# Kernel tuning notes

Hardware: AMD Instinct MI355X
Metric: run time of the kernel (lower is better)

The kernel has to match this reference:

```python
import jax, jax.numpy as jnp
import numpy as np
from jax import lax

WS = 8       # RSA window size
HEADS = 8    # GSA heads
EPS_LN = 1e-5

def conv1x1(x, w):  # x:(b,c,h,w), w:(o,c)
    return jnp.einsum('bchw,oc->bohw', x, w)

def dwconv3x3(x, w):  # w:(c,1,3,3) depthwise
    return lax.conv_general_dilated(x, w, (1, 1), ((1, 1), (1, 1)),
                                    dimension_numbers=('NCHW', 'OIHW', 'NCHW'),
                                    feature_group_count=x.shape[1])

def layernorm(x, w, b):  # WithBias LayerNorm over channel dim
    mu = x.mean(axis=1, keepdims=True)
    var = ((x - mu) ** 2).mean(axis=1, keepdims=True)
    return (x - mu) / jnp.sqrt(var + EPS_LN) * w[None, :, None, None] + b[None, :, None, None]

def l2norm(x):  # F.normalize(dim=-1)
    n = jnp.sqrt(jnp.sum(x * x, axis=-1, keepdims=True))
    return x / jnp.maximum(n, 1e-12)

def window_part(x, ws):  # (b,c,H,W) -> (b,nwin,ws*ws,c)
    b, c, H, W = x.shape
    x = x.reshape(b, c, H // ws, ws, W // ws, ws)
    x = x.transpose(0, 2, 4, 3, 5, 1)
    return x.reshape(b, (H // ws) * (W // ws), ws * ws, c)

def window_merge(x, ws, H, W):  # inverse of window_part
    b, nwin, _, c = x.shape
    x = x.reshape(b, H // ws, W // ws, ws, ws, c)
    x = x.transpose(0, 5, 1, 3, 2, 4)
    return x.reshape(b, c, H, W)

def rsa(x, qkv_w, dw_w, proj_w, temp):
    b, c, H, W = x.shape
    sh = WS // 2  # torch: roll by -wsize//2 = -4
    x_ = jnp.roll(x, (-sh, -sh), axis=(2, 3))
    qkv = dwconv3x3(conv1x1(x_, qkv_w), dw_w)
    q, k, v = jnp.split(qkv, 3, axis=1)
    q = l2norm(window_part(q, WS))
    k = l2norm(window_part(k, WS))
    v = window_part(v, WS)
    # attn[c,d] = sum_p q[p,c] k[p,d]; relu instead of softmax
    attn = jax.nn.relu(jnp.einsum('bnpc,bnpd->bncd', q, k) * temp[0, 0, 0])
    out = jnp.einsum('bnpc,bncd->bnpd', v, attn)
    out = window_merge(out, WS, H, W)
    out = jnp.roll(out, (sh, sh), axis=(2, 3))
    return conv1x1(out, proj_w), attn

def gsa(x, qkv_w, dw_w, proj_w, temp):
    b, c, H, W = x.shape
    cp = c // HEADS
    qkv = dwconv3x3(conv1x1(x, qkv_w), dw_w)
    q, k, v = jnp.split(qkv, 3, axis=1)
    heads = lambda t: t.reshape(b, HEADS, cp, H * W)
    q = l2norm(heads(q)); k = l2norm(heads(k)); v = heads(v)
    attn = jax.nn.relu(jnp.einsum('bhcn,bhdn->bhcd', q, k) * temp[0, 0, 0])
    out = jnp.einsum('bhcd,bhdn->bhcn', attn, v)  # (b,head,cp,HW)
    # rearrange 'b head c hw -> b (head c) h w' then 'b (head c) h w -> b (c head) h w'
    y = out.reshape(b, HEADS, cp, H, W).transpose(0, 2, 1, 3, 4).reshape(b, c, H, W)
    return conv1x1(y, proj_w), attn

def ffn(x, in_w, dw_w, out_w):  # Restormer gated-dconv FFN, bias=False
    h2 = dwconv3x3(conv1x1(x, in_w), dw_w)
    x1, x2 = jnp.split(h2, 2, axis=1)
    return conv1x1(jax.nn.gelu(x1, approximate=False) * x2, out_w)


def setup_inputs() -> dict:
    key = jax.random.key(0)
    B, C, H, W = 8, 64, 128, 128
    HID = int(C * 2.66)  # 170
    ks = jax.random.split(key, 20)
    g = lambda k, shp, s: (jax.random.normal(k, shp, dtype=jnp.float32) * s)
    d = {
        'x': g(ks[0], (B, C, H, W), 1.0),
        'ln_s0_w': jnp.ones((C,), jnp.float32), 'ln_s0_b': jnp.zeros((C,), jnp.float32),
        'ln_s2_w': jnp.ones((C,), jnp.float32), 'ln_s2_b': jnp.zeros((C,), jnp.float32),
        'rsa_qkv_w': g(ks[1], (3 * C, C), 0.05), 'rsa_dw_w': g(ks[2], (3 * C, 1, 3, 3), 0.1),
        'rsa_proj_w': g(ks[3], (C, C), 0.05), 'rsa_temp': jnp.ones((1, 1, 1), jnp.float32),
        'ffd_s_in_w': g(ks[4], (2 * HID, C), 0.05), 'ffd_s_dw_w': g(ks[5], (2 * HID, 1, 3, 3), 0.1),
        'ffd_s_out_w': g(ks[6], (C, HID), 0.05),
        'ln_c0_w': jnp.ones((C,), jnp.float32), 'ln_c0_b': jnp.zeros((C,), jnp.float32),
        'ln_c2_w': jnp.ones((C,), jnp.float32), 'ln_c2_b': jnp.zeros((C,), jnp.float32),
        'gsa_qkv_w': g(ks[7], (3 * C, C), 0.05), 'gsa_dw_w': g(ks[8], (3 * C, 1, 3, 3), 0.1),
        'gsa_proj_w': g(ks[9], (C, C), 0.05), 'gsa_temp': jnp.ones((1, 1, 1), jnp.float32),
        'ffd_c_in_w': g(ks[10], (2 * HID, C), 0.05), 'ffd_c_dw_w': g(ks[11], (2 * HID, 1, 3, 3), 0.1),
        'ffd_c_out_w': g(ks[12], (C, HID), 0.05),
    }
    return d


def reference(x, ln_s0_w, ln_s0_b, ln_s2_w, ln_s2_b,
              rsa_qkv_w, rsa_dw_w, rsa_proj_w, rsa_temp,
              ffd_s_in_w, ffd_s_dw_w, ffd_s_out_w,
              ln_c0_w, ln_c0_b, ln_c2_w, ln_c2_b,
              gsa_qkv_w, gsa_dw_w, gsa_proj_w, gsa_temp,
              ffd_c_in_w, ffd_c_dw_w, ffd_c_out_w):
    # FDT block, shared_depth=1 (i==0 branches only)
    x_, _ = rsa(layernorm(x, ln_s0_w, ln_s0_b), rsa_qkv_w, rsa_dw_w, rsa_proj_w, rsa_temp)
    x = ffn(layernorm(x_ + x, ln_s2_w, ln_s2_b), ffd_s_in_w, ffd_s_dw_w, ffd_s_out_w) + x_
    x_, _ = gsa(layernorm(x, ln_c0_w, ln_c0_b), gsa_qkv_w, gsa_dw_w, gsa_proj_w, gsa_temp)
    x = ffn(layernorm(x_ + x, ln_c2_w, ln_c2_b), ffd_c_in_w, ffd_c_dw_w, ffd_c_out_w) + x_
    return x
```

## Files before the change

kernel.cpp:

```cpp
#include <hip/hip_runtime.h>
#include <hip/hip_bf16.h>
#include <math.h>

#define DI __device__ __forceinline__

constexpr int B = 8, C = 64, H = 128, W = 128, N = H * W;
constexpr int HID = 170;
constexpr int QKVC = 3 * C;

typedef _Float16 half8 __attribute__((ext_vector_type(8)));
typedef _Float16 half4v __attribute__((ext_vector_type(4)));
typedef float f32x4 __attribute__((ext_vector_type(4)));

extern "C" __device__ _Float16 __ocml_exp_f16(_Float16);

DI half8 gelu_gate_h8(half8 a, half8 g) {
    const _Float16 k = (_Float16)0.044715f;
    const _Float16 c = (_Float16)1.5957691f;
    half8 a2 = a * a;
    half8 t = a * ((_Float16)1.f + k * a2);
    half8 o;
#pragma unroll
    for (int i = 0; i < 8; ++i) {
        _Float16 e = __ocml_exp_f16((_Float16)(-c * t[i]));
        o[i] = (_Float16)(a[i] / ((_Float16)1.f + e) * g[i]);
    }
    return o;
}

DI void wpack_dev(const float* __restrict__ Wm, const float* __restrict__ lnsc,
                  int OREAL, int KREAL, int KT, _Float16* __restrict__ out,
                  int f, int l)
{
    int mt = f / KT, kt = f % KT;
    int row = mt * 16 + (l & 15);
    int col0 = kt * 32 + (l >> 4) * 8;
    half8 v;
#pragma unroll
    for (int i = 0; i < 8; ++i) {
        int col = col0 + i;
        float w = (row < OREAL && col < KREAL) ? Wm[row * KREAL + col] : 0.f;
        if (lnsc && col < KREAL) w *= lnsc[col];
        v[i] = (_Float16)w;
    }
    *(half8*)(out + (size_t)f * 512 + l * 8) = v;
}

DI void wbias_dev(const float* __restrict__ Wm, const float* __restrict__ lnb,
                  int OREAL, int OPAD, float* __restrict__ biasv, int blk, int l)
{
    int o = blk * 64 + l;
    if (o >= OPAD) return;
    float s = 0.f;
    if (o < OREAL) {
#pragma unroll
        for (int c = 0; c < 64; ++c) s += Wm[o * 64 + c] * lnb[c];
    }
    biasv[o] = s;
}

__global__ __launch_bounds__(64) void prep_kernel(
    const float* rsa_qkv_w, const float* ln_s0_w, const float* ln_s0_b,
    const float* gsa_qkv_w, const float* ln_c0_w, const float* ln_c0_b,
    const float* ffs_in_w,  const float* ln_s2_w, const float* ln_s2_b,
    const float* ffc_in_w,  const float* ln_c2_w, const float* ln_c2_b,
    const float* ffs_out_w, const float* ffc_out_w, const float* rsa_proj_w,
    _Float16* wp_rsa, _Float16* wp_gsa, _Float16* wp_fsi, _Float16* wp_fci,
    _Float16* wp_fso, _Float16* wp_fco, _Float16* wp_rsap,
    float* wb_rsa, float* wb_gsa, float* wb_fsi, float* wb_fci)
{
    int bid = blockIdx.x, l = threadIdx.x;
    if      (bid < 24)  wpack_dev(rsa_qkv_w, ln_s0_w, 192, 64, 2, wp_rsa, bid, l);
    else if (bid < 48)  wpack_dev(gsa_qkv_w, ln_c0_w, 192, 64, 2, wp_gsa, bid - 24, l);
    else if (bid < 96)  wpack_dev(ffs_in_w,  ln_s2_w, 340, 64, 2, wp_fsi, bid - 48, l);
    else if (bid < 144) wpack_dev(ffc_in_w,  ln_c2_w, 340, 64, 2, wp_fci, bid - 96, l);
    else if (bid < 168) wpack_dev(ffs_out_w, nullptr, 64, 170, 6, wp_fso, bid - 144, l);
    else if (bid < 192) wpack_dev(ffc_out_w, nullptr, 64, 170, 6, wp_fco, bid - 168, l);
    else if (bid < 200) wpack_dev(rsa_proj_w, nullptr, 64, 64, 2, wp_rsap, bid - 192, l);
    else if (bid < 203) wbias_dev(rsa_qkv_w, ln_s0_b, 192, 192, wb_rsa, bid - 200, l);
    else if (bid < 206) wbias_dev(gsa_qkv_w, ln_c0_b, 192, 192, wb_gsa, bid - 203, l);
    else if (bid < 212) wbias_dev(ffs_in_w, ln_s2_b, 340, 384, wb_fsi, bid - 206, l);
    else                wbias_dev(ffc_in_w, ln_c2_b, 340, 384, wb_fci, bid - 212, l);
}

__global__ __launch_bounds__(256, 1) void xpose_kernel(
    const float* __restrict__ x, _Float16* __restrict__ xT)
{
    __shared__ _Float16 tile[64][72];
    int blk = blockIdx.x;
    int b = blk >> 8, tb = blk & 255;
    int n0 = tb * 64;
    int t = threadIdx.x;
    {
        int ch = t >> 2, seg = t & 3;
        const float* xp = x + ((size_t)b * 64 + ch) * N + n0 + seg * 16;
#pragma unroll
        for (int jj = 0; jj < 4; ++jj) {
            f32x4 v = *(const f32x4*)(xp + jj * 4);
#pragma unroll
            for (int k = 0; k < 4; ++k)
                tile[seg * 16 + jj * 4 + k][ch] = (_Float16)v[k];
        }
    }
    __syncthreads();
    {
        int px = t >> 2, part = t & 3;
        half8 h0 = *(const half8*)&tile[px][part * 16];
        half8 h1 = *(const half8*)&tile[px][part * 16 + 8];
        _Float16* op = xT + ((size_t)b * N + n0 + px) * 64 + part * 16;
        *(half8*)op = h0;
        *(half8*)(op + 8) = h1;
    }
}

template<int MT, int OREAL, bool ADDIN>
__global__ __launch_bounds__(512, 1) void lngemm_kernel(
    const _Float16* __restrict__ Xp, const _Float16* __restrict__ Rp,
    const float* __restrict__ biasv,
    const _Float16* __restrict__ Wp, _Float16* __restrict__ outp)
{
    __shared__ _Float16 stash[4][MT][16][66];
    int t = threadIdx.x, lane = t & 63, wv = t >> 6;
    int mg = wv & 3, ph = wv >> 2;
    int pbase = blockIdx.x * 64;
    int b = pbase >> 14, nb = pbase & (N - 1);
    int g = lane >> 4, lm = lane & 15;
    int krow0 = g * 8;

    half8 a[MT][2];
    const _Float16* wb = Wp + (size_t)(mg * MT * 2) * 512 + lane * 8;
#pragma unroll
    for (int mt = 0; mt < MT; ++mt)
#pragma unroll
        for (int kt = 0; kt < 2; ++kt)
            a[mt][kt] = *(const half8*)(wb + (mt * 2 + kt) * 512);

    int rowbase = mg * (MT * 16);
    const float* bp = biasv + rowbase + g * 4;

    const _Float16* xb = Xp + (size_t)b * N * 64;
    const _Float16* ab = ADDIN ? (Rp + (size_t)b * N * 64) : nullptr;

#pragma unroll
    for (int cg2 = 0; cg2 < 2; ++cg2) {
        int cg = ph * 2 + cg2;
        int col = nb + cg * 16 + lm;
        const _Float16* xp = xb + (size_t)col * 64;
        half8 h0 = *(const half8*)(xp + krow0);
        half8 h1 = *(const half8*)(xp + 32 + krow0);
        float vv[2][8];
        float sm = 0.f, ss = 0.f;
        if (ADDIN) {
            const _Float16* ap = ab + (size_t)col * 64;
            half8 r0 = *(const half8*)(ap + krow0);
            half8 r1 = *(const half8*)(ap + 32 + krow0);
#pragma unroll
            for (int i = 0; i < 8; ++i) {
                float v0 = (float)h0[i] + (float)r0[i];
                float v1 = (float)h1[i] + (float)r1[i];
                vv[0][i] = v0; vv[1][i] = v1;
                sm += v0 + v1; ss += v0 * v0 + v1 * v1;
            }
        } else {
#pragma unroll
            for (int i = 0; i < 8; ++i) {
                float v0 = (float)h0[i], v1 = (float)h1[i];
                vv[0][i] = v0; vv[1][i] = v1;
                sm += v0 + v1; ss += v0 * v0 + v1 * v1;
            }
        }
        sm += __shfl_xor(sm, 16); ss += __shfl_xor(ss, 16);
        sm += __shfl_xor(sm, 32); ss += __shfl_xor(ss, 32);
        float mu = sm * (1.0f / 64.0f);
        float var = ss * (1.0f / 64.0f) - mu * mu;
        float rstd = rsqrtf(var + 1e-5f);
        half8 bf[2];
#pragma unroll
        for (int kt = 0; kt < 2; ++kt)
#pragma unroll
            for (int i = 0; i < 8; ++i)
                bf[kt][i] = (_Float16)((vv[kt][i] - mu) * rstd);

        f32x4 acc[MT];
#pragma unroll
        for (int mt = 0; mt < MT; ++mt) acc[mt] = *(const f32x4*)(bp + mt * 16);
#pragma unroll
        for (int kt = 0; kt < 2; ++kt)
#pragma unroll
            for (int mt = 0; mt < MT; ++mt)
                acc[mt] = __builtin_amdgcn_mfma_f32_16x16x32_f16(a[mt][kt], bf[kt], acc[mt], 0, 0, 0);

#pragma unroll
        for (int mt = 0; mt < MT; ++mt)
#pragma unroll
            for (int r = 0; r < 4; ++r)
                stash[mg][mt][g * 4 + r][cg * 16 + lm] = (_Float16)acc[mt][r];
    }
    __syncthreads();

    int tid128 = ph * 64 + lane;
    int row = tid128 >> 3, ch8 = tid128 & 7;
#pragma unroll
    for (int mt = 0; mt < MT; ++mt) {
        int orow = rowbase + mt * 16 + row;
        if ((4 * MT * 16 == OREAL) || orow < OREAL) {
            half8 v0 = *(const half8*)&stash[mg][mt][row][ch8 * 8];
            *(half8*)(outp + ((size_t)b * OREAL + orow) * N + nb + ch8 * 8) = v0;
        }
    }
}

template<int MT, int KT, int MG, int NSTRIP, int CIN, int OREAL, int XROWS,
         bool PBW, bool OUT32, bool RESID>
__global__ __launch_bounds__(256, 1) void gemm_kernel(
    const _Float16* __restrict__ X, const _Float16* __restrict__ Wp,
    const _Float16* __restrict__ resid, void* __restrict__ outv)
{
    constexpr int PG = 4 / MG;
    constexpr int PPB = PG * 16 * NSTRIP;
    int t = threadIdx.x;
    int lane = t & 63, wv = t >> 6;
    int mg = wv % MG, pg = wv / MG;
    int pbase = blockIdx.x * PPB;
    int b = pbase >> 14, nb = pbase & (N - 1);

    half8 a[MT][KT];
    const _Float16* wb = Wp + ((size_t)(PBW ? b * (MG * MT * KT) : 0) + mg * MT * KT) * 512 + lane * 8;
#pragma unroll
    for (int mt = 0; mt < MT; ++mt)
#pragma unroll
        for (int kt = 0; kt < KT; ++kt)
            a[mt][kt] = *(const half8*)(wb + (mt * KT + kt) * 512);

    const _Float16* xb = X + (size_t)b * XROWS * N;
    int krow0 = (lane >> 4) * 8;

    for (int s = 0; s < NSTRIP; ++s) {
        int col = nb + (s * PG + pg) * 16 + (lane & 15);
        const _Float16* xp = xb + col;
        half8 bf[KT];
#pragma unroll
        for (int kt = 0; kt < KT; ++kt)
#pragma unroll
            for (int i = 0; i < 8; ++i) {
                int c = kt * 32 + krow0 + i;
                if (KT * 32 <= CIN || c < CIN) bf[kt][i] = xp[(size_t)c * N];
                else bf[kt][i] = (_Float16)0.f;
            }
        f32x4 acc[MT];
#pragma unroll
        for (int mt = 0; mt < MT; ++mt) acc[mt] = (f32x4){0.f, 0.f, 0.f, 0.f};
#pragma unroll
        for (int kt = 0; kt < KT; ++kt)
#pragma unroll
            for (int mt = 0; mt < MT; ++mt)
                acc[mt] = __builtin_amdgcn_mfma_f32_16x16x32_f16(a[mt][kt], bf[kt], acc[mt], 0, 0, 0);

        int orow0 = mg * (MT * 16) + (lane >> 4) * 4;
#pragma unroll
        for (int mt = 0; mt < MT; ++mt) {
            int ob0 = orow0 + mt * 16;
            half4v res;
            if constexpr (RESID)
                res = *(const half4v*)(resid + ((size_t)b * N + col) * 64 + ob0);
            if constexpr (OUT32) {
#pragma unroll
                for (int r = 0; r < 4; ++r) {
                    float vv = acc[mt][r];
                    if constexpr (RESID) vv += (float)res[r];
                    ((float*)outv)[((size_t)b * OREAL + ob0 + r) * N + col] = vv;
                }
            } else {
                half4v h;
#pragma unroll
                for (int r = 0; r < 4; ++r) {
                    float vv = acc[mt][r];
                    if constexpr (RESID) vv += (float)res[r];
                    h[r] = (_Float16)vv;
                }
                *(half4v*)((_Float16*)outv + ((size_t)b * N + col) * 64 + ob0) = h;
            }
        }
    }
}

template<bool ROLLWM>
__global__ __launch_bounds__(256, 1) void dw16_kernel(
    const _Float16* __restrict__ in, const float* __restrict__ w,
    _Float16* __restrict__ out)
{
    int bc = blockIdx.y;
    int c = bc % 192;
    int n0 = (blockIdx.x * 256 + threadIdx.x) * 8;
    int y = n0 >> 7, x0 = n0 & 127;
    const _Float16* ib = in + (size_t)bc * N;
    const float* wr = w + c * 9;
    _Float16 wh[9];
#pragma unroll
    for (int i = 0; i < 9; ++i) wh[i] = (_Float16)wr[i];

    half8 acc = {0, 0, 0, 0, 0, 0, 0, 0};
#pragma unroll
    for (int r = 0; r < 3; ++r) {
        int yy = y - 1 + r;
        if (yy < 0 || yy > 127) continue;
        half8 sL, m, sR;
        if (!ROLLWM) {
            const _Float16* rp = ib + yy * W + x0;
            m = *(const half8*)rp;
            half8 pv = {0, 0, 0, 0, 0, 0, 0, 0};
            half8 nv = {0, 0, 0, 0, 0, 0, 0, 0};
            pv[7] = (x0 > 0) ? rp[-1] : (_Float16)0.f;
            nv[0] = (x0 < 120) ? rp[8] : (_Float16)0.f;
            sL = __builtin_shufflevector(pv, m, 7, 8, 9, 10, 11, 12, 13, 14);
            sR = __builtin_shufflevector(m, nv, 1, 2, 3, 4, 5, 6, 7, 8);
        } else {
            int sy = (yy + 4) & 127;
            const _Float16* rp = ib + sy * W;
            if (x0 <= 112) {
                half8 b0 = *(const half8*)(rp + x0);
                half8 b1 = *(const half8*)(rp + x0 + 8);
                sL = __builtin_shufflevector(b0, b1, 3, 4, 5, 6, 7, 8, 9, 10);
                m  = __builtin_shufflevector(b0, b1, 4, 5, 6, 7, 8, 9, 10, 11);
                sR = __builtin_shufflevector(b0, b1, 5, 6, 7, 8, 9, 10, 11, 12);
                if (x0 == 0) sL[0] = (_Float16)0.f;
            } else {
                _Float16 tmp[10];
#pragma unroll
                for (int j = 0; j < 10; ++j) {
                    int xx = 119 + j;
                    tmp[j] = (xx <= 127) ? rp[(xx + 4) & 127] : (_Float16)0.f;
                }
#pragma unroll
                for (int j = 0; j < 8; ++j) { sL[j] = tmp[j]; m[j] = tmp[j + 1]; sR[j] = tmp[j + 2]; }
            }
        }
        acc += sL * wh[r * 3 + 0] + m * wh[r * 3 + 1] + sR * wh[r * 3 + 2];
    }
    if (ROLLWM) {
        int win = ((y >> 3) << 4) | (x0 >> 3);
        int p = (y & 7) << 3;
        *(half8*)(out + (size_t)bc * N + win * 64 + p) = acc;
    } else {
        *(half8*)(out + (size_t)bc * N + n0) = acc;
    }
}

__global__ __launch_bounds__(256, 3) void rsa_win_kernel(
    const _Float16* __restrict__ qkv, const float* __restrict__ temp_p,
    const _Float16* __restrict__ pwp, _Float16* __restrict__ out)
{
    __shared__ _Float16 qT[64][72];
    __shared__ _Float16 kT[64][72];
    __shared__ _Float16 vP[64][76];
    __shared__ _Float16 aT[64][76];
    __shared__ _Float16 oP[64][76];
    __shared__ float tnorm[128];
    __shared__ _Float16 wsc[64];
    int blk = blockIdx.x, b = blk >> 8, win = blk & 255;
    int t = threadIdx.x, lane = t & 63, wv = t >> 6;
    int g = lane >> 4, lm = lane & 15;

    half8 pa0 = *(const half8*)(pwp + (size_t)(wv * 2 + 0) * 512 + lane * 8);
    half8 pa1 = *(const half8*)(pwp + (size_t)(wv * 2 + 1) * 512 + lane * 8);

    const _Float16* base = qkv + (size_t)b * QKVC * N + win * 64;
    {
        int c = t >> 2, q0 = (t & 3) * 16;
        const _Float16* pq = base + (size_t)c * N + q0;
        half8 a0 = *(const half8*)(pq);
        half8 a1 = *(const half8*)(pq + 8);
        *(half8*)&qT[c][q0] = a0;
        *(half8*)&qT[c][q0 + 8] = a1;
        const _Float16* pk = base + (size_t)(64 + c) * N + q0;
        half8 b0 = *(const half8*)(pk);
        half8 b1 = *(const half8*)(pk + 8);
        *(half8*)&kT[c][q0] = b0;
        *(half8*)&kT[c][q0 + 8] = b1;
        const _Float16* pv = base + (size_t)(128 + c) * N + q0;
        half8 v0 = *(const half8*)(pv);
        half8 v1 = *(const half8*)(pv + 8);
#pragma unroll
        for (int j = 0; j < 8; ++j) vP[q0 + j][c] = v0[j];
#pragma unroll
        for (int j = 0; j < 8; ++j) vP[q0 + 8 + j][c] = v1[j];
    }
    __syncthreads();
    if (t < 128) {
        int p = t & 63;
        float s = 0.f;
        if (t < 64) {
#pragma unroll
            for (int c = 0; c < 64; ++c) { float a = (float)qT[c][p]; s += a * a; }
        } else {
#pragma unroll
            for (int c = 0; c < 64; ++c) { float a = (float)kT[c][p]; s += a * a; }
        }
        tnorm[t] = s;
    }
    __syncthreads();
    if (t < 64) {
        float r = temp_p[0] / (fmaxf(sqrtf(tnorm[t]), 1e-12f) * fmaxf(sqrtf(tnorm[64 + t]), 1e-12f));
        wsc[t] = (_Float16)r;
    }
    __syncthreads();

    {
        half8 aq0 = *(const half8*)&qT[wv * 16 + lm][g * 8];
        half8 aq1 = *(const half8*)&qT[wv * 16 + lm][32 + g * 8];
        half8 ws0 = *(const half8*)&wsc[g * 8];
        half8 ws1 = *(const half8*)&wsc[32 + g * 8];
#pragma unroll
        for (int nt = 0; nt < 4; ++nt) {
            int d = nt * 16 + lm;
            half8 bk0 = *(const half8*)&kT[d][g * 8] * ws0;
            half8 bk1 = *(const half8*)&kT[d][32 + g * 8] * ws1;
            f32x4 acc = {0.f, 0.f, 0.f, 0.f};
            acc = __builtin_amdgcn_mfma_f32_16x16x32_f16(aq0, bk0, acc, 0, 0, 0);
            acc = __builtin_amdgcn_mfma_f32_16x16x32_f16(aq1, bk1, acc, 0, 0, 0);
#pragma unroll
            for (int r = 0; r < 4; ++r)
                aT[wv * 16 + g * 4 + r][d] = (_Float16)fmaxf(acc[r], 0.f);
        }
    }
    __syncthreads();

    {
        half8 a20, a21;
#pragma unroll
        for (int i = 0; i < 8; ++i) {
            a20[i] = aT[g * 8 + i][wv * 16 + lm];
            a21[i] = aT[32 + g * 8 + i][wv * 16 + lm];
        }
#pragma unroll
        for (int nt = 0; nt < 4; ++nt) {
            int p = nt * 16 + lm;
            half4v x0 = *(const half4v*)&vP[p][g * 8];
            half4v x1 = *(const half4v*)&vP[p][g * 8 + 4];
            half4v x2 = *(const half4v*)&vP[p][32 + g * 8];
            half4v x3 = *(const half4v*)&vP[p][32 + g * 8 + 4];
            half8 b20, b21;
#pragma unroll
            for (int j = 0; j < 4; ++j) { b20[j] = x0[j]; b20[4 + j] = x1[j]; b21[j] = x2[j]; b21[4 + j] = x3[j]; }
            f32x4 acc = {0.f, 0.f, 0.f, 0.f};
            acc = __builtin_amdgcn_mfma_f32_16x16x32_f16(a20, b20, acc, 0, 0, 0);
            acc = __builtin_amdgcn_mfma_f32_16x16x32_f16(a21, b21, acc, 0, 0, 0);
#pragma unroll
            for (int r = 0; r < 4; ++r)
                oP[p][wv * 16 + g * 4 + r] = (_Float16)acc[r];
        }
    }
    __syncthreads();

    {
        int y0 = (win >> 4) * 8, x0w = (win & 15) * 8;
        _Float16* ob = out + (size_t)b * N * 64;
#pragma unroll
        for (int nt = 0; nt < 4; ++nt) {
            int p = nt * 16 + lm;
            half4v x0 = *(const half4v*)&oP[p][g * 8];
            half4v x1 = *(const half4v*)&oP[p][g * 8 + 4];
            half4v x2 = *(const half4v*)&oP[p][32 + g * 8];
            half4v x3 = *(const half4v*)&oP[p][32 + g * 8 + 4];
            half8 b30, b31;
#pragma unroll
            for (int j = 0; j < 4; ++j) { b30[j] = x0[j]; b30[4 + j] = x1[j]; b31[j] = x2[j]; b31[4 + j] = x3[j]; }
            f32x4 acc = {0.f, 0.f, 0.f, 0.f};
            acc = __builtin_amdgcn_mfma_f32_16x16x32_f16(pa0, b30, acc, 0, 0, 0);
            acc = __builtin_amdgcn_mfma_f32_16x16x32_f16(pa1, b31, acc, 0, 0, 0);
            int gy = (y0 + (p >> 3) + 4) & 127;
            int gx = (x0w + (p & 7) + 4) & 127;
            half4v h;
#pragma unroll
            for (int r = 0; r < 4; ++r) h[r] = (_Float16)acc[r];
            *(half4v*)(ob + (size_t)(gy * W + gx) * 64 + wv * 16 + g * 4) = h;
        }
    }
}

__global__ __launch_bounds__(256, 1) void ffn_b_kernel(
    const _Float16* __restrict__ hid,
    const float* __restrict__ dww,
    _Float16* __restrict__ gated)
{
    int c = blockIdx.y, b = blockIdx.z;
    int n0 = (blockIdx.x * 256 + threadIdx.x) * 8;
    int y = n0 >> 7, x0 = n0 & 127;
    const _Float16* pa = hid + ((size_t)b * 340 + c) * N;
    const _Float16* pb = pa + (size_t)170 * N;
    const float* wa = dww + c * 9;
    const float* wbp = wa + 170 * 9;
    _Float16 wha[9], whb[9];
#pragma unroll
    for (int i = 0; i < 9; ++i) { wha[i] = (_Float16)wa[i]; whb[i] = (_Float16)wbp[i]; }

    half8 accA = {0, 0, 0, 0, 0, 0, 0, 0};
    half8 accB = {0, 0, 0, 0, 0, 0, 0, 0};
#pragma unroll
    for (int r = 0; r < 3; ++r) {
        int yy = y - 1 + r;
        if (yy < 0 || yy > 127) continue;
        {
            const _Float16* ra = pa + yy * W + x0;
            half8 m = *(const half8*)ra;
            half8 pv = {0, 0, 0, 0, 0, 0, 0, 0};
            half8 nv = {0, 0, 0, 0, 0, 0, 0, 0};
            pv[7] = (x0 > 0) ? ra[-1] : (_Float16)0.f;
            nv[0] = (x0 < 120) ? ra[8] : (_Float16)0.f;
            half8 sL = __builtin_shufflevector(pv, m, 7, 8, 9, 10, 11, 12, 13, 14);
            half8 sR = __builtin_shufflevector(m, nv, 1, 2, 3, 4, 5, 6, 7, 8);
            accA += sL * wha[r * 3 + 0] + m * wha[r * 3 + 1] + sR * wha[r * 3 + 2];
        }
        {
            const _Float16* rb = pb + yy * W + x0;
            half8 m = *(const half8*)rb;
            half8 pv = {0, 0, 0, 0, 0, 0, 0, 0};
            half8 nv = {0, 0, 0, 0, 0, 0, 0, 0};
            pv[7] = (x0 > 0) ? rb[-1] : (_Float16)0.f;
            nv[0] = (x0 < 120) ? rb[8] : (_Float16)0.f;
            half8 sL = __builtin_shufflevector(pv, m, 7, 8, 9, 10, 11, 12, 13, 14);
            half8 sR = __builtin_shufflevector(m, nv, 1, 2, 3, 4, 5, 6, 7, 8);
            accB += sL * whb[r * 3 + 0] + m * whb[r * 3 + 1] + sR * whb[r * 3 + 2];
        }
    }
    *(half8*)(gated + ((size_t)b * 170 + c) * N + n0) = gelu_gate_h8(accA, accB);
}

__global__ __launch_bounds__(256, 1) void gsa_part_kernel(
    const _Float16* __restrict__ qkv, float* __restrict__ part)
{
    int bh = blockIdx.y, chunk = blockIdx.x;
    int b = bh >> 3, h = bh & 7;
    int t = threadIdx.x;
    const _Float16* qb = qkv + ((size_t)b * QKVC + h * 8) * N;
    const _Float16* kb = qb + (size_t)64 * N;
    float acc[80];
#pragma unroll
    for (int j = 0; j < 80; ++j) acc[j] = 0.f;
    for (int i = 0; i < 8; ++i) {
        int n = chunk * 2048 + i * 256 + t;
        float qv[8], kv[8];
#pragma unroll
        for (int c = 0; c < 8; ++c) { qv[c] = (float)qb[(size_t)c * N + n]; kv[c] = (float)kb[(size_t)c * N + n]; }
#pragma unroll
        for (int c = 0; c < 8; ++c) {
            acc[64 + c] += qv[c] * qv[c];
            acc[72 + c] += kv[c] * kv[c];
#pragma unroll
            for (int d = 0; d < 8; ++d) acc[c * 8 + d] += qv[c] * kv[d];
        }
    }
#pragma unroll
    for (int j = 0; j < 80; ++j) {
        float v = acc[j];
#pragma unroll
        for (int m = 1; m < 64; m <<= 1) v += __shfl_xor(v, m, 64);
        acc[j] = v;
    }
    __shared__ float red[4 * 80];
    if ((t & 63) == 0) {
#pragma unroll
        for (int j = 0; j < 80; ++j) red[(t >> 6) * 80 + j] = acc[j];
    }
    __syncthreads();
    if (t < 80) {
        float s = red[t] + red[80 + t] + red[160 + t] + red[240 + t];
        part[((size_t)bh * 8 + chunk) * 80 + t] = s;
    }
}

__global__ __launch_bounds__(512) void gsa_fin2_kernel(
    const float* __restrict__ part, const float* __restrict__ temp_p,
    const float* __restrict__ pw, _Float16* __restrict__ wp_pbw)
{
    __shared__ float al[512];
    int b = blockIdx.x, tid = threadIdx.x;
    int h = tid >> 6, t64 = tid & 63;
    {
        int bh = b * 8 + h;
        int c = t64 >> 3, d = t64 & 7;
        float S = 0.f, q2 = 0.f, k2 = 0.f;
#pragma unroll
        for (int ch = 0; ch < 8; ++ch) {
            const float* p = part + ((size_t)bh * 8 + ch) * 80;
            S += p[t64]; q2 += p[64 + c]; k2 += p[72 + d];
        }
        float qn = fmaxf(sqrtf(q2), 1e-12f);
        float kn = fmaxf(sqrtf(k2), 1e-12f);
        al[h * 64 + t64] = fmaxf(temp_p[0] * S / (qn * kn), 0.f);
    }
    __syncthreads();
    int f = tid >> 6, l = tid & 63;
    int mt = f >> 1, kt = f & 1;
    int row = mt * 16 + (l & 15);
    int col0 = kt * 32 + (l >> 4) * 8;
    half8 v;
#pragma unroll
    for (int i = 0; i < 8; ++i) {
        int col = col0 + i;
        int hh = col >> 3, dd = col & 7;
        float acc = 0.f;
#pragma unroll
        for (int cc = 0; cc < 8; ++cc)
            acc += pw[row * 64 + cc * 8 + hh] * al[hh * 64 + cc * 8 + dd];
        v[i] = (_Float16)acc;
    }
    *(half8*)(wp_pbw + ((size_t)b * 8 + f) * 512 + l * 8) = v;
}

__global__ void sentinel_kernel(float* out, int n) {
    int i = blockIdx.x * 256 + threadIdx.x;
    if (i < n) out[i] = 12345.0f;
}

extern "C" void kernel_launch(void* const* d_in, const int* in_sizes, int n_in,
                              void* d_out, int out_size, void* d_ws, size_t ws_size,
                              hipStream_t stream)
{
    const float* x         = (const float*)d_in[0];
    const float* ln_s0_w   = (const float*)d_in[1];
    const float* ln_s0_b   = (const float*)d_in[2];
    const float* ln_s2_w   = (const float*)d_in[3];
    const float* ln_s2_b   = (const float*)d_in[4];
    const float* rsa_qkv_w = (const float*)d_in[5];
    const float* rsa_dw_w  = (const float*)d_in[6];
    const float* rsa_proj_w= (const float*)d_in[7];
    const float* rsa_temp  = (const float*)d_in[8];
    const float* ffs_in_w  = (const float*)d_in[9];
    const float* ffs_dw_w  = (const float*)d_in[10];
    const float* ffs_out_w = (const float*)d_in[11];
    const float* ln_c0_w   = (const float*)d_in[12];
    const float* ln_c0_b   = (const float*)d_in[13];
    const float* ln_c2_w   = (const float*)d_in[14];
    const float* ln_c2_b   = (const float*)d_in[15];
    const float* gsa_qkv_w = (const float*)d_in[16];
    const float* gsa_dw_w  = (const float*)d_in[17];
    const float* gsa_proj_w= (const float*)d_in[18];
    const float* gsa_temp  = (const float*)d_in[19];
    const float* ffc_in_w  = (const float*)d_in[20];
    const float* ffc_dw_w  = (const float*)d_in[21];
    const float* ffc_out_w = (const float*)d_in[22];
    float* outp = (float*)d_out;

    char* ws = (char*)d_ws;
    _Float16* tmp192 = (_Float16*)(ws + 0);
    _Float16* Qbuf16 = (_Float16*)(ws + 50331648ull);
    _Float16* hidA   = (_Float16*)(ws + 0);
    _Float16* gated  = (_Float16*)(ws + 89128960ull);
    _Float16* wp_rsap= (_Float16*)(ws + 133693440ull);
    _Float16* S2h    = (_Float16*)(ws + 134217728ull);
    _Float16* X2h    = (_Float16*)(ws + 150994944ull);
    _Float16* xT     = X2h;
    float*    part   = (float*)(ws + 167772160ull);
    _Float16* wp_rsa = (_Float16*)(ws + 168574976ull);
    _Float16* wp_gsa = (_Float16*)(ws + 168599552ull);
    _Float16* wp_fsi = (_Float16*)(ws + 168624128ull);
    _Float16* wp_fci = (_Float16*)(ws + 168673280ull);
    _Float16* wp_fso = (_Float16*)(ws + 168722432ull);
    _Float16* wp_fco = (_Float16*)(ws + 168747008ull);
    _Float16* wp_pbw = (_Float16*)(ws + 168771584ull);
    float*    wb_rsa = (float*)(ws + 168837120ull);
    float*    wb_gsa = (float*)(ws + 168838144ull);
    float*    wb_fsi = (float*)(ws + 168839168ull);
    float*    wb_fci = (float*)(ws + 168841216ull);
    if (ws_size < 168843264ull) {
        int n = out_size < 4096 ? out_size : 4096;
        sentinel_kernel<<<16, 256, 0, stream>>>(outp, n);
        return;
    }

    dim3 blk256(256), blk512(512);

    prep_kernel<<<218, 64, 0, stream>>>(
        rsa_qkv_w, ln_s0_w, ln_s0_b,
        gsa_qkv_w, ln_c0_w, ln_c0_b,
        ffs_in_w,  ln_s2_w, ln_s2_b,
        ffc_in_w,  ln_c2_w, ln_c2_b,
        ffs_out_w, ffc_out_w, rsa_proj_w,
        wp_rsa, wp_gsa, wp_fsi, wp_fci, wp_fso, wp_fco, wp_rsap,
        wb_rsa, wb_gsa, wb_fsi, wb_fci);

    xpose_kernel<<<2048, blk256, 0, stream>>>(x, xT);
    lngemm_kernel<3, 192, false><<<2048, blk512, 0, stream>>>(xT, nullptr, wb_rsa, wp_rsa, tmp192);
    dw16_kernel<true><<<dim3(8, B * 192), blk256, 0, stream>>>(tmp192, rsa_dw_w, Qbuf16);
    rsa_win_kernel<<<2048, blk256, 0, stream>>>(Qbuf16, rsa_temp, wp_rsap, S2h);
    lngemm_kernel<6, 340, true><<<2048, blk512, 0, stream>>>(S2h, xT, wb_fsi, wp_fsi, hidA);
    ffn_b_kernel<<<dim3(8, 170, B), blk256, 0, stream>>>(hidA, ffs_dw_w, gated);
    gemm_kernel<2, 6, 2, 2, 170, 64, 170, false, false, true>
        <<<2048, blk256, 0, stream>>>(gated, wp_fso, S2h, X2h);

    lngemm_kernel<3, 192, false><<<2048, blk512, 0, stream>>>(X2h, nullptr, wb_gsa, wp_gsa, tmp192);
    dw16_kernel<false><<<dim3(8, B * 192), blk256, 0, stream>>>(tmp192, gsa_dw_w, Qbuf16);
    gsa_part_kernel<<<dim3(8, 64), blk256, 0, stream>>>(Qbuf16, part);
    gsa_fin2_kernel<<<8, blk512, 0, stream>>>(part, gsa_temp, gsa_proj_w, wp_pbw);
    gemm_kernel<4, 2, 1, 1, 64, 64, 192, true, false, false>
        <<<2048, blk256, 0, stream>>>(Qbuf16 + (size_t)128 * N, wp_pbw, nullptr, S2h);
    lngemm_kernel<6, 340, true><<<2048, blk512, 0, stream>>>(S2h, X2h, wb_fci, wp_fci, hidA);
    ffn_b_kernel<<<dim3(8, 170, B), blk256, 0, stream>>>(hidA, ffc_dw_w, gated);
    gemm_kernel<2, 6, 2, 2, 170, 64, 170, false, true, true>
        <<<2048, blk256, 0, stream>>>(gated, wp_fco, S2h, outp);
}
```

Baseline: 354.2 us.

## Fuse FFN depthwise conv and GELU gate into output projection GEMM

Replaces the separate depthwise-3x3 + GELU-gating kernel and the following 170->64 projection GEMM with a single kernel per FFN. Each block computes the gated hidden activations for a 64-pixel row segment into shared memory, then runs MFMA against the projection weights and adds the residual. This removes the write and re-read of the 170-channel gated intermediate and one launch per FFN. In exchange, the LDS B-operand gather is scalar and possibly bank-conflicted, occupancy is limited by the 22KB shared buffer, and the rows above and below are loaded per block with no reuse across neighbouring rows.

```diff
diff --git a/kernel.cpp b/kernel.cpp
--- a/kernel.cpp
+++ b/kernel.cpp
@@ -278,6 +278,126 @@
                     if constexpr (RESID) vv += (float)res[r];
                     h[r] = (_Float16)vv;
                 }
+                *(half4v*)((_Float16*)outv + ((size_t)b * N + col) * 64 + ob0) = h;
+            }
+        }
+    }
+}
+
+template<bool OUT32>
+__global__ __launch_bounds__(256, 1) void ffngemm_kernel(
+    const _Float16* __restrict__ hid,
+    const float* __restrict__ dww,
+    const _Float16* __restrict__ Wp,
+    const _Float16* __restrict__ resid,
+    void* __restrict__ outv)
+{
+    __shared__ _Float16 glds[170][66];
+    int t = threadIdx.x;
+    int pbase = blockIdx.x * 64;
+    int b = pbase >> 14, nb = pbase & (N - 1);
+    int y = nb >> 7, x00 = nb & 127;
+
+    for (int idx = t; idx < 680; idx += 256) {
+        int c = idx >> 2, q = idx & 3;
+        int xq = x00 + q * 16;
+        const float* wa = dww + c * 9;
+        const float* wbp = wa + 170 * 9;
+        _Float16 wha[9], whb[9];
+#pragma unroll
+        for (int i = 0; i < 9; ++i) { wha[i] = (_Float16)wa[i]; whb[i] = (_Float16)wbp[i]; }
+        const _Float16* pa = hid + ((size_t)b * 340 + c) * N + y * W + xq;
+        const _Float16* pb = pa + (size_t)170 * N;
+        half8 aA0 = {0,0,0,0,0,0,0,0}, aA1 = {0,0,0,0,0,0,0,0};
+        half8 aB0 = {0,0,0,0,0,0,0,0}, aB1 = {0,0,0,0,0,0,0,0};
+#pragma unroll
+        for (int r = 0; r < 3; ++r) {
+            int yy = y - 1 + r;
+            if (yy < 0 || yy > 127) continue;
+            int ro = (r - 1) * W;
+            {
+                const _Float16* ra = pa + ro;
+                half8 m0 = *(const half8*)ra;
+                half8 m1 = *(const half8*)(ra + 8);
+                half8 pv = {0,0,0,0,0,0,0,0};
+                half8 nv = {0,0,0,0,0,0,0,0};
+                pv[7] = (xq > 0)   ? ra[-1] : (_Float16)0.f;
+                nv[0] = (xq < 112) ? ra[16] : (_Float16)0.f;
+                half8 sL0 = __builtin_shufflevector(pv, m0, 7, 8, 9, 10, 11, 12, 13, 14);
+                half8 sR0 = __builtin_shufflevector(m0, m1, 1, 2, 3, 4, 5, 6, 7, 8);
+                half8 sL1 = __builtin_shufflevector(m0, m1, 7, 8, 9, 10, 11, 12, 13, 14);
+                half8 sR1 = __builtin_shufflevector(m1, nv, 1, 2, 3, 4, 5, 6, 7, 8);
+                aA0 += sL0 * wha[r * 3 + 0] + m0 * wha[r * 3 + 1] + sR0 * wha[r * 3 + 2];
+                aA1 += sL1 * wha[r * 3 + 0] + m1 * wha[r * 3 + 1] + sR1 * wha[r * 3 + 2];
+            }
+            {
+                const _Float16* rb = pb + ro;
+                half8 m0 = *(const half8*)rb;
+                half8 m1 = *(const half8*)(rb + 8);
+                half8 pv = {0,0,0,0,0,0,0,0};
+                half8 nv = {0,0,0,0,0,0,0,0};
+                pv[7] = (xq > 0)   ? rb[-1] : (_Float16)0.f;
+                nv[0] = (xq < 112) ? rb[16] : (_Float16)0.f;
+                half8 sL0 = __builtin_shufflevector(pv, m0, 7, 8, 9, 10, 11, 12, 13, 14);
+                half8 sR0 = __builtin_shufflevector(m0, m1, 1, 2, 3, 4, 5, 6, 7, 8);
+                half8 sL1 = __builtin_shufflevector(m0, m1, 7, 8, 9, 10, 11, 12, 13, 14);
+                half8 sR1 = __builtin_shufflevector(m1, nv, 1, 2, 3, 4, 5, 6, 7, 8);
+                aB0 += sL0 * whb[r * 3 + 0] + m0 * whb[r * 3 + 1] + sR0 * whb[r * 3 + 2];
+                aB1 += sL1 * whb[r * 3 + 0] + m1 * whb[r * 3 + 1] + sR1 * whb[r * 3 + 2];
+            }
+        }
+        half8 g0 = gelu_gate_h8(aA0, aB0);
+        half8 g1 = gelu_gate_h8(aA1, aB1);
+        *(half8*)&glds[c][q * 16] = g0;
+        *(half8*)&glds[c][q * 16 + 8] = g1;
+    }
+    __syncthreads();
+
+    int lane = t & 63, wv = t >> 6;
+    int mg = wv & 1, pg = wv >> 1;
+    half8 a[2][6];
+    const _Float16* wb = Wp + (size_t)(mg * 12) * 512 + lane * 8;
+#pragma unroll
+    for (int mt = 0; mt < 2; ++mt)
+#pragma unroll
+        for (int kt = 0; kt < 6; ++kt)
+            a[mt][kt] = *(const half8*)(wb + (mt * 6 + kt) * 512);
+    int krow0 = (lane >> 4) * 8;
+
+#pragma unroll
+    for (int s = 0; s < 2; ++s) {
+        int colL = (s * 2 + pg) * 16 + (lane & 15);
+        int col = nb + colL;
+        half8 bf[6];
+#pragma unroll
+        for (int kt = 0; kt < 6; ++kt)
+#pragma unroll
+            for (int i = 0; i < 8; ++i) {
+                int c = kt * 32 + krow0 + i;
+                bf[kt][i] = (c < 170) ? glds[c][colL] : (_Float16)0.f;
+            }
+        f32x4 acc[2];
+        acc[0] = (f32x4){0.f, 0.f, 0.f, 0.f};
+        acc[1] = (f32x4){0.f, 0.f, 0.f, 0.f};
+#pragma unroll
+        for (int kt = 0; kt < 6; ++kt)
+#pragma unroll
+            for (int mt = 0; mt < 2; ++mt)
+                acc[mt] = __builtin_amdgcn_mfma_f32_16x16x32_f16(a[mt][kt], bf[kt], acc[mt], 0, 0, 0);
+
+        int orow0 = mg * 32 + (lane >> 4) * 4;
+#pragma unroll
+        for (int mt = 0; mt < 2; ++mt) {
+            int ob0 = orow0 + mt * 16;
+            half4v res = *(const half4v*)(resid + ((size_t)b * N + col) * 64 + ob0);
+            if constexpr (OUT32) {
+#pragma unroll
+                for (int r = 0; r < 4; ++r)
+                    ((float*)outv)[((size_t)b * 64 + ob0 + r) * N + col] = acc[mt][r] + (float)res[r];
+            } else {
+                half4v h;
+#pragma unroll
+                for (int r = 0; r < 4; ++r) h[r] = (_Float16)(acc[mt][r] + (float)res[r]);
                 *(half4v*)((_Float16*)outv + ((size_t)b * N + col) * 64 + ob0) = h;
             }
         }
@@ -478,54 +598,6 @@
     }
 }
 
-__global__ __launch_bounds__(256, 1) void ffn_b_kernel(
-    const _Float16* __restrict__ hid,
-    const float* __restrict__ dww,
-    _Float16* __restrict__ gated)
-{
-    int c = blockIdx.y, b = blockIdx.z;
-    int n0 = (blockIdx.x * 256 + threadIdx.x) * 8;
-    int y = n0 >> 7, x0 = n0 & 127;
-    const _Float16* pa = hid + ((size_t)b * 340 + c) * N;
-    const _Float16* pb = pa + (size_t)170 * N;
-    const float* wa = dww + c * 9;
-    const float* wbp = wa + 170 * 9;
-    _Float16 wha[9], whb[9];
-#pragma unroll
-    for (int i = 0; i < 9; ++i) { wha[i] = (_Float16)wa[i]; whb[i] = (_Float16)wbp[i]; }
-
-    half8 accA = {0, 0, 0, 0, 0, 0, 0, 0};
-    half8 accB = {0, 0, 0, 0, 0, 0, 0, 0};
-#pragma unroll
-    for (int r = 0; r < 3; ++r) {
-        int yy = y - 1 + r;
-        if (yy < 0 || yy > 127) continue;
-        {
-            const _Float16* ra = pa + yy * W + x0;
-            half8 m = *(const half8*)ra;
-            half8 pv = {0, 0, 0, 0, 0, 0, 0, 0};
-            half8 nv = {0, 0, 0, 0, 0, 0, 0, 0};
-            pv[7] = (x0 > 0) ? ra[-1] : (_Float16)0.f;
-            nv[0] = (x0 < 120) ? ra[8] : (_Float16)0.f;
-            half8 sL = __builtin_shufflevector(pv, m, 7, 8, 9, 10, 11, 12, 13, 14);
-            half8 sR = __builtin_shufflevector(m, nv, 1, 2, 3, 4, 5, 6, 7, 8);
-            accA += sL * wha[r * 3 + 0] + m * wha[r * 3 + 1] + sR * wha[r * 3 + 2];
-        }
-        {
-            const _Float16* rb = pb + yy * W + x0;
-            half8 m = *(const half8*)rb;
-            half8 pv = {0, 0, 0, 0, 0, 0, 0, 0};
-            half8 nv = {0, 0, 0, 0, 0, 0, 0, 0};
-            pv[7] = (x0 > 0) ? rb[-1] : (_Float16)0.f;
-            nv[0] = (x0 < 120) ? rb[8] : (_Float16)0.f;
-            half8 sL = __builtin_shufflevector(pv, m, 7, 8, 9, 10, 11, 12, 13, 14);
-            half8 sR = __builtin_shufflevector(m, nv, 1, 2, 3, 4, 5, 6, 7, 8);
-            accB += sL * whb[r * 3 + 0] + m * whb[r * 3 + 1] + sR * whb[r * 3 + 2];
-        }
-    }
-    *(half8*)(gated + ((size_t)b * 170 + c) * N + n0) = gelu_gate_h8(accA, accB);
-}
-
 __global__ __launch_bounds__(256, 1) void gsa_part_kernel(
     const _Float16* __restrict__ qkv, float* __restrict__ part)
 {
@@ -646,7 +718,6 @@
     _Float16* tmp192 = (_Float16*)(ws + 0);
     _Float16* Qbuf16 = (_Float16*)(ws + 50331648ull);
     _Float16* hidA   = (_Float16*)(ws + 0);
-    _Float16* gated  = (_Float16*)(ws + 89128960ull);
     _Float16* wp_rsap= (_Float16*)(ws + 133693440ull);
     _Float16* S2h    = (_Float16*)(ws + 134217728ull);
     _Float16* X2h    = (_Float16*)(ws + 150994944ull);
@@ -685,9 +756,7 @@
     dw16_kernel<true><<<dim3(8, B * 192), blk256, 0, stream>>>(tmp192, rsa_dw_w, Qbuf16);
     rsa_win_kernel<<<2048, blk256, 0, stream>>>(Qbuf16, rsa_temp, wp_rsap, S2h);
     lngemm_kernel<6, 340, true><<<2048, blk512, 0, stream>>>(S2h, xT, wb_fsi, wp_fsi, hidA);
-    ffn_b_kernel<<<dim3(8, 170, B), blk256, 0, stream>>>(hidA, ffs_dw_w, gated);
-    gemm_kernel<2, 6, 2, 2, 170, 64, 170, false, false, true>
-        <<<2048, blk256, 0, stream>>>(gated, wp_fso, S2h, X2h);
+    ffngemm_kernel<false><<<2048, blk256, 0, stream>>>(hidA, ffs_dw_w, wp_fso, S2h, X2h);
 
     lngemm_kernel<3, 192, false><<<2048, blk512, 0, stream>>>(X2h, nullptr, wb_gsa, wp_gsa, tmp192);
     dw16_kernel<false><<<dim3(8, B * 192), blk256, 0, stream>>>(tmp192, gsa_dw_w, Qbuf16);
@@ -696,7 +765,5 @@
     gemm_kernel<4, 2, 1, 1, 64, 64, 192, true, false, false>
         <<<2048, blk256, 0, stream>>>(Qbuf16 + (size_t)128 * N, wp_pbw, nullptr, S2h);
     lngemm_kernel<6, 340, true><<<2048, blk512, 0, stream>>>(S2h, X2h, wb_fci, wp_fci, hidA);
-    ffn_b_kernel<<<dim3(8, 170, B), blk256, 0, stream>>>(hidA, ffc_dw_w, gated);
-    gemm_kernel<2, 6, 2, 2, 170, 64, 170, false, true, true>
-        <<<2048, blk256, 0, stream>>>(gated, wp_fco, S2h, outp);
-}
+    ffngemm_kernel<true><<<2048, blk256, 0, stream>>>(hidA, ffc_dw_w, wp_fco, S2h, outp);
+}
```

Measured after the change: 394.0 us. 11.2% more time.
